# Kernel tuning notes

Hardware: AMD Instinct MI355X
Metric: run time of the kernel (lower is better)

The kernel has to match this reference:

```python
import jax, jax.numpy as jnp
import numpy as np

B, D = 512, 512
NOBJ, NWRD = 12, 16  # word_feat rows act as 'objects', object_feat rows as 'words' (arg swap in SentiGAT.forward)
N_OW = NOBJ + NWRD
EPS = 1e-12


def _with_self_loops(src, dst, n):
    return (np.concatenate([src, np.arange(n)]), np.concatenate([dst, np.arange(n)]))

_src = np.tile(np.arange(NOBJ), NWRD)                 # arange(n_obj).repeat(n_words) in torch == tile
_dst = np.repeat(np.arange(NWRD), NOBJ) + NOBJ        # repeat_interleave + offset
SRC_OW, DST_OW = map(jnp.asarray, _with_self_loops(_src, _dst, N_OW))

_E5 = np.array([[0,0,0,0,1,1,1,1,2,2,2,2,3,3,3,3,4,4,4,4],
                [1,2,3,4,0,2,3,4,0,1,3,4,0,1,2,4,0,1,2,3]])
SRC5, DST5 = map(jnp.asarray, _with_self_loops(_E5[0], _E5[1], 5))


def gat_conv(x, src, dst, W, a_src, a_dst, bias, concat, num_nodes):
    """PyG GATConv (add_self_loops already in src/dst, negative_slope=0.2, dropout=0)."""
    heads, out_dim = a_src.shape
    h = (x @ W).reshape(num_nodes, heads, out_dim)
    e = jax.nn.leaky_relu((h * a_src).sum(-1)[src] + (h * a_dst).sum(-1)[dst], 0.2)  # [E, heads]
    m = jax.ops.segment_max(e, dst, num_segments=num_nodes)
    p = jnp.exp(e - m[dst])
    alpha = p / jax.ops.segment_sum(p, dst, num_segments=num_nodes)[dst]             # softmax over incoming edges
    out = jax.ops.segment_sum(alpha[:, :, None] * h[src], dst, num_segments=num_nodes)
    out = out.reshape(num_nodes, heads * out_dim) if concat else out.mean(axis=1)
    return out + bias


def _ind_norm(f):
    # add_feature_indicator + F.normalize(p=2, dim=1, eps=1e-12)
    v = (f.sum(axis=1) != 0).astype(f.dtype)[:, None]
    g = jnp.concatenate([f, v], axis=1)
    return g / jnp.maximum(jnp.linalg.norm(g, axis=1, keepdims=True), EPS)


def setup_inputs() -> dict:
    k = jax.random.split(jax.random.key(0), 32)
    r = lambda i, s: jax.random.normal(k[i], s, dtype=jnp.float32)
    sc = 0.05
    return {
        "text_feat": r(0, (B, D)), "image_feat": r(1, (B, D)), "imgtxt_feat": r(2, (B, D)),
        "face_feat": r(3, (B, D)), "word_feat": r(4, (B, NOBJ, D)), "object_feat": r(5, (B, NWRD, D)),
        "ow_W": r(6, (D, 2 * D)) * sc, "ow_asrc": r(7, (2, D)) * sc, "ow_adst": r(8, (2, D)) * sc,
        "ow_b": jnp.zeros((D,), jnp.float32),
        "g1_W": r(9, (D + 1, D)) * sc, "g1_asrc": r(10, (1, D)) * sc, "g1_adst": r(11, (1, D)) * sc,
        "g1_b": jnp.zeros((D,), jnp.float32),
        "g2_W": r(12, (D, D)) * sc, "g2_asrc": r(13, (1, D)) * sc, "g2_adst": r(14, (1, D)) * sc,
        "g2_b": jnp.zeros((D,), jnp.float32),
        "m1_W": r(15, (5 * D, D)) * sc, "m1_b": jnp.zeros((D,), jnp.float32),
        "m2_W": r(16, (D, 3)) * sc, "m2_b": jnp.zeros((3,), jnp.float32),
    }


def reference(text_feat, image_feat, imgtxt_feat, face_feat, word_feat, object_feat,
              ow_W, ow_asrc, ow_adst, ow_b,
              g1_W, g1_asrc, g1_adst, g1_b,
              g2_W, g2_asrc, g2_adst, g2_b,
              m1_W, m1_b, m2_W, m2_b):
    # --- ObjectWordGAT (object_embs=word_feat, word_embs=object_feat per SentiGAT.forward) ---
    def per_sample(obj, wrd):
        x = jnp.concatenate([obj, wrd], axis=0)                       # [N_OW, D]
        h = gat_conv(x, SRC_OW, DST_OW, ow_W, ow_asrc, ow_adst, ow_b, False, N_OW)
        uo, uw = h[:NOBJ], h[NOBJ:]
        attn = jax.nn.softmax(uo @ uw.T, axis=1)                      # [NOBJ, NWRD]
        return (attn @ uw).mean(axis=0)                               # [D]
    aligned = jax.vmap(per_sample)(word_feat, object_feat)            # [B, D]

    feats = [_ind_norm(f) for f in (text_feat, image_feat, imgtxt_feat, face_feat, aligned)]
    x = jnp.stack(feats, axis=1)                                      # [B, 5, D+1]

    # edge_attr (cosine sims) is ignored by GATConv when edge_dim is None
    def graph5(xb):
        h = gat_conv(xb, SRC5, DST5, g1_W, g1_asrc, g1_adst, g1_b, True, 5)
        h = jax.nn.relu(h)
        return gat_conv(h, SRC5, DST5, g2_W, g2_asrc, g2_adst, g2_b, True, 5)
    x = jax.vmap(graph5)(x)                                           # [B, 5, D]

    fused = x.reshape(B, 5 * D)
    hid = jax.nn.relu(fused @ m1_W + m1_b)                            # dropout = identity (eval)
    return hid @ m2_W + m2_b                                          # [B, 3] logits
```

## Files before the change

### kernel.cpp

```cpp
#include <hip/hip_runtime.h>
#include <hip/hip_bf16.h>
#include <math.h>


#define B_SAMP 512

typedef short short8 __attribute__((ext_vector_type(8)));
typedef float floatx4 __attribute__((ext_vector_type(4)));

__device__ __forceinline__ float lrelu02(float x) { return x > 0.f ? x : 0.2f * x; }

__device__ __forceinline__ unsigned short cvt_bf16(float f) {
    union { float f; unsigned int u; } v; v.f = f;
    unsigned int u = v.u;
    return (unsigned short)((u + 0x7FFFu + ((u >> 16) & 1u)) >> 16);
}

__global__ __launch_bounds__(256) void prep(
    const float* __restrict__ ow_W, const float* __restrict__ ow_asrc,
    const float* __restrict__ ow_adst,
    const float* __restrict__ g1_W, const float* __restrict__ g2_W,
    const float* __restrict__ m1_W,
    float* __restrict__ vg, unsigned short* __restrict__ owWt,
    unsigned short* __restrict__ g1Wt, unsigned short* __restrict__ g2Wt,
    unsigned short* __restrict__ m1Wt)
{
    __shared__ float T[32][33];
    const int tid = threadIdx.x;
    int bid = blockIdx.x;

    if (bid < 128) {
        const int lane = tid & 63;
        const int gw = bid * 4 + (tid >> 6);
        for (int idx = gw; idx < 2048; idx += 512) {
            int t = idx >> 9, k = idx & 511;
            const float* a = (t < 2) ? (ow_asrc + t * 512) : (ow_adst + (t - 2) * 512);
            const float* wr = ow_W + (size_t)k * 1024 + (t & 1) * 512;
            float s = 0.f;
#pragma unroll
            for (int j = 0; j < 8; ++j) s += wr[lane + 64 * j] * a[lane + 64 * j];
            for (int off = 32; off > 0; off >>= 1) s += __shfl_down(s, off, 64);
            if (lane == 0) vg[idx] = s;
        }
        return;
    }
    bid -= 128;
    const float* W; int ldw, K, Kpad, koff, ktiles; float scale; unsigned short* Wt;
    if (bid < 256)        { W = ow_W;       ldw = 1024; K = 512;  Kpad = 1024; koff = 0;   scale = 0.5f; Wt = owWt; ktiles = 16; }
    else if (bid < 512)   { bid -= 256;  W = ow_W + 512; ldw = 1024; K = 512;  Kpad = 1024; koff = 512; scale = 0.5f; Wt = owWt; ktiles = 16; }
    else if (bid < 784)   { bid -= 512;  W = g1_W; ldw = 512; K = 513;  Kpad = 544;  koff = 0; scale = 1.f; Wt = g1Wt; ktiles = 17; }
    else if (bid < 1040)  { bid -= 784;  W = g2_W; ldw = 512; K = 512;  Kpad = 512;  koff = 0; scale = 1.f; Wt = g2Wt; ktiles = 16; }
    else                  { bid -= 1040; W = m1_W; ldw = 512; K = 2560; Kpad = 2560; koff = 0; scale = 1.f; Wt = m1Wt; ktiles = 80; }
    const int k0 = (bid % ktiles) * 32;
    const int n0 = (bid / ktiles) * 32;
    {
        int kr = tid >> 3, nc = (tid & 7) * 4;
        float4 v = make_float4(0.f, 0.f, 0.f, 0.f);
        if (k0 + kr < K) v = *(const float4*)(W + (size_t)(k0 + kr) * ldw + n0 + nc);
        T[nc + 0][kr] = v.x * scale; T[nc + 1][kr] = v.y * scale;
        T[nc + 2][kr] = v.z * scale; T[nc + 3][kr] = v.w * scale;
    }
    __syncthreads();
    {
        int nr = tid >> 3, kc = (tid & 7) * 4;
        ushort4 w;
        w.x = cvt_bf16(T[nr][kc + 0]);
        w.y = cvt_bf16(T[nr][kc + 1]);
        w.z = cvt_bf16(T[nr][kc + 2]);
        w.w = cvt_bf16(T[nr][kc + 3]);
        *(ushort4*)(Wt + (size_t)(n0 + nr) * Kpad + koff + k0 + kc) = w;
    }
}

__global__ __launch_bounds__(256) void ow_pre(
    const float* __restrict__ wf, const float* __restrict__ of,
    const float* __restrict__ vg,
    unsigned short* __restrict__ zcat)
{
    const int b = blockIdx.x;
    __shared__ float Xs[28][512];
    __shared__ float ss[28][2], sd[28][2];
    __shared__ float alpha[16][2][13];

    const int tid = threadIdx.x;
    const int lane = tid & 63;
    const int wid = tid >> 6;

    for (int idx = tid; idx < 28 * 128; idx += 256) {
        int n = idx >> 7, c = (idx & 127) * 4;
        const float* src = (n < 12) ? (wf + ((size_t)b * 12 + n) * 512)
                                    : (of + ((size_t)b * 16 + (n - 12)) * 512);
        *(float4*)&Xs[n][c] = *(const float4*)(src + c);
    }
    __syncthreads();

    for (int p = wid; p < 112; p += 4) {
        int n = p >> 2, t = p & 3;
        const float* vv = vg + t * 512;
        float s = 0.f;
#pragma unroll
        for (int j = 0; j < 8; ++j) s += Xs[n][lane + 64 * j] * vv[lane + 64 * j];
        for (int off = 32; off > 0; off >>= 1) s += __shfl_down(s, off, 64);
        if (lane == 0) { if (t < 2) ss[n][t] = s; else sd[n][t - 2] = s; }
    }
    __syncthreads();

    if (tid < 32) {
        int w = tid >> 1, h = tid & 1;
        float sdv = sd[12 + w][h];
        float e[13];
        float mx = -1e30f;
        for (int j = 0; j < 12; ++j) {
            e[j] = lrelu02(ss[j][h] + sdv);
            mx = fmaxf(mx, e[j]);
        }
        e[12] = lrelu02(ss[12 + w][h] + sdv);
        mx = fmaxf(mx, e[12]);
        float den = 0.f;
        for (int j = 0; j < 13; ++j) { e[j] = expf(e[j] - mx); den += e[j]; }
        float inv = 1.f / den;
        for (int j = 0; j < 13; ++j) alpha[w][h][j] = e[j] * inv;
    }
    __syncthreads();

    unsigned short* zb = zcat + (size_t)b * 28 * 1024;
    for (int idx = tid; idx < 12 * 1024; idx += 256) {
        int n = idx >> 10, d = idx & 511;
        zb[idx] = cvt_bf16(Xs[n][d]);
    }
    for (int c = tid; c < 1024; c += 256) {
        int h = c >> 9, d = c & 511;
        float xr[12];
#pragma unroll
        for (int j = 0; j < 12; ++j) xr[j] = Xs[j][d];
#pragma unroll 4
        for (int w = 0; w < 16; ++w) {
            float a = alpha[w][h][12] * Xs[12 + w][d];
#pragma unroll
            for (int j = 0; j < 12; ++j) a += alpha[w][h][j] * xr[j];
            zb[(size_t)(12 + w) * 1024 + c] = cvt_bf16(a);
        }
    }
}

template <int BM, int BN, int RELU, int SPLITK>
__global__ __launch_bounds__(256) void gemm_v2(
    const unsigned short* __restrict__ A, int lda,
    const unsigned short* __restrict__ Bt, int ldbt,
    float* __restrict__ C, int ldc,
    int M, int N, int K,
    const float* __restrict__ bias)
{
    constexpr int WM = BM / 2, WN = BN / 2;
    constexpr int MF = WM / 16, NF = WN / 16;
    constexpr int CA = BM / 64, CB = BN / 64;

    __shared__ unsigned short As[2][BM][40];
    __shared__ unsigned short Bs[2][BN][40];

    const int tid = threadIdx.x;
    const int m0 = blockIdx.x * BM;
    const int n0 = blockIdx.y * BN;
    const int lane = tid & 63;
    const int wid = tid >> 6;
    const int wm = (wid & 1) * WM;
    const int wn = (wid >> 1) * WN;
    const int fr = lane & 15;
    const int kq = (lane >> 4) * 8;

    const int srow = tid >> 2;
    const int scol = (tid & 3) * 8;

    const int kchunk = K / SPLITK;
    const int kbeg = (SPLITK > 1) ? blockIdx.z * kchunk : 0;
    const int kend = kbeg + kchunk;
    if (SPLITK > 1) C += (size_t)blockIdx.z * M * ldc;

    short8 ra[CA], rb[CB];
#define LOADAB(K0)                                                                   \
    do {                                                                             \
        _Pragma("unroll")                                                            \
        for (int c = 0; c < CA; ++c)                                                 \
            ra[c] = *(const short8*)(A + (size_t)(m0 + srow + c * 64) * lda + (K0) + scol); \
        _Pragma("unroll")                                                            \
        for (int c = 0; c < CB; ++c)                                                 \
            rb[c] = *(const short8*)(Bt + (size_t)(n0 + srow + c * 64) * ldbt + (K0) + scol); \
    } while (0)

    LOADAB(kbeg);

    floatx4 acc[MF][NF];
#pragma unroll
    for (int i = 0; i < MF; ++i)
#pragma unroll
        for (int j = 0; j < NF; ++j) acc[i][j] = (floatx4){0.f, 0.f, 0.f, 0.f};

    int t = 0;
    for (int k0 = kbeg; k0 < kend; k0 += 32, t ^= 1) {
#pragma unroll
        for (int c = 0; c < CA; ++c) *(short8*)&As[t][srow + c * 64][scol] = ra[c];
#pragma unroll
        for (int c = 0; c < CB; ++c) *(short8*)&Bs[t][srow + c * 64][scol] = rb[c];
        __syncthreads();
        if (k0 + 32 < kend) LOADAB(k0 + 32);

        short8 af[MF], bw[NF];
#pragma unroll
        for (int i = 0; i < MF; ++i)
            af[i] = *(const short8*)&As[t][wm + i * 16 + fr][kq];
#pragma unroll
        for (int j = 0; j < NF; ++j)
            bw[j] = *(const short8*)&Bs[t][wn + j * 16 + fr][kq];
#pragma unroll
        for (int i = 0; i < MF; ++i)
#pragma unroll
            for (int j = 0; j < NF; ++j)
                acc[i][j] = __builtin_amdgcn_mfma_f32_16x16x32_bf16(
                    af[i], bw[j], acc[i][j], 0, 0, 0);
    }
#undef LOADAB

    const int fq = lane >> 4;
#pragma unroll
    for (int i = 0; i < MF; ++i) {
#pragma unroll
        for (int j = 0; j < NF; ++j) {
#pragma unroll
            for (int q = 0; q < 4; ++q) {
                int row = m0 + wm + i * 16 + fq * 4 + q;
                int col = n0 + wn + j * 16 + fr;
                float v = acc[i][j][q];
                if (SPLITK == 1 && bias) v += bias[col];
                if (RELU) v = fmaxf(v, 0.f);
                C[(size_t)row * ldc + col] = v;
            }
        }
    }
}

__global__ __launch_bounds__(256) void attn_x5(
    const float* __restrict__ hout,
    const float* __restrict__ tf, const float* __restrict__ im,
    const float* __restrict__ it, const float* __restrict__ fa,
    unsigned short* __restrict__ x5)
{
    const int b = blockIdx.x;
    __shared__ float uo[12][520];
    __shared__ float uw[16][520];
    __shared__ float S[12][16];
    __shared__ float w16[16];
    __shared__ float al[512];

    const int tid = threadIdx.x;
    const int lane = tid & 63;
    const int wave = tid >> 6;
    const float* hb = hout + (size_t)b * 28 * 512;

    for (int idx = tid; idx < 28 * 128; idx += 256) {
        int n = idx >> 7, c = (idx & 127) * 4;
        float* row = (n < 12) ? &uo[n][0] : &uw[n - 12][0];
        *(float4*)&row[c] = *(const float4*)(hb + (size_t)n * 512 + c);
    }
    __syncthreads();

    if (tid < 192) {
        int i = tid >> 4, j = tid & 15;
        float s = 0.f;
        for (int d = 0; d < 128; ++d) {
            float4 a = *(const float4*)&uo[i][d * 4];
            float4 c = *(const float4*)&uw[j][d * 4];
            s += a.x * c.x + a.y * c.y + a.z * c.z + a.w * c.w;
        }
        S[i][j] = s;
    }
    __syncthreads();

    if (tid < 12) {
        float mx = -1e30f;
        for (int j = 0; j < 16; ++j) mx = fmaxf(mx, S[tid][j]);
        float den = 0.f;
        for (int j = 0; j < 16; ++j) { float p = expf(S[tid][j] - mx); S[tid][j] = p; den += p; }
        float inv = 1.f / den;
        for (int j = 0; j < 16; ++j) S[tid][j] *= inv;
    }
    __syncthreads();

    if (tid < 16) {
        float s = 0.f;
        for (int i = 0; i < 12; ++i) s += S[i][tid];
        w16[tid] = s * (1.f / 12.f);
    }
    __syncthreads();

    for (int d = tid; d < 512; d += 256) {
        float s = 0.f;
#pragma unroll
        for (int j = 0; j < 16; ++j) s += w16[j] * uw[j][d];
        al[d] = s;
    }
    __syncthreads();

    for (int f = wave; f < 5; f += 4) {
        const float* src = (f == 0) ? tf : (f == 1) ? im : (f == 2) ? it : (f == 3) ? fa : nullptr;
        float vals[8];
        float sum = 0.f, sq = 0.f;
#pragma unroll
        for (int j = 0; j < 8; ++j) {
            float v = (f < 4) ? src[(size_t)b * 512 + lane + 64 * j] : al[lane + 64 * j];
            vals[j] = v;
            sum += v;
            sq += v * v;
        }
#pragma unroll
        for (int off = 32; off > 0; off >>= 1) {
            sum += __shfl_xor(sum, off, 64);
            sq  += __shfl_xor(sq,  off, 64);
        }
        float v = (sum != 0.f) ? 1.f : 0.f;
        float nrm = fmaxf(sqrtf(sq + v * v), 1e-12f);
        float inv = 1.f / nrm;
        unsigned short* dst = x5 + ((size_t)b * 5 + f) * 544;
#pragma unroll
        for (int j = 0; j < 8; ++j) dst[lane + 64 * j] = cvt_bf16(vals[j] * inv);
        if (lane == 0) dst[512] = cvt_bf16(v * inv);
        else if (lane < 32) dst[512 + lane] = 0;
    }
}

template <int RELU>
__global__ __launch_bounds__(256) void g5_gat(
    const float* __restrict__ Hg,
    const float* __restrict__ asrc, const float* __restrict__ adst,
    const float* __restrict__ bias, unsigned short* __restrict__ outp)
{
    const int b = blockIdx.x;
    __shared__ float ss[5], sd[5];
    __shared__ float alpha[5][5];

    const int tid = threadIdx.x;
    const int lane = tid & 63;
    const int wave = tid >> 6;
    const float* Hb = Hg + (size_t)b * 5 * 512;

    for (int p = wave; p < 10; p += 4) {
        int n = p >> 1, ty = p & 1;
        const float* hv = Hb + n * 512;
        const float* av = ty ? adst : asrc;
        float s = 0.f;
#pragma unroll
        for (int j = 0; j < 8; ++j) s += hv[lane + 64 * j] * av[lane + 64 * j];
        for (int off = 32; off > 0; off >>= 1) s += __shfl_down(s, off, 64);
        if (lane == 0) { if (ty) sd[n] = s; else ss[n] = s; }
    }
    __syncthreads();

    if (tid < 5) {
        int dn = tid;
        float e[5];
        float mx = -1e30f;
        for (int s = 0; s < 5; ++s) {
            e[s] = lrelu02(ss[s] + sd[dn]);
            mx = fmaxf(mx, e[s]);
        }
        float den = 0.f;
        for (int s = 0; s < 5; ++s) { e[s] = expf(e[s] - mx); den += e[s]; }
        float inv = 1.f / den;
        for (int s = 0; s < 5; ++s) alpha[dn][s] = e[s] * inv;
    }
    __syncthreads();

    for (int d = tid; d < 512; d += 256) {
        float h0 = Hb[0 * 512 + d], h1 = Hb[1 * 512 + d], h2 = Hb[2 * 512 + d];
        float h3 = Hb[3 * 512 + d], h4 = Hb[4 * 512 + d];
        float bd = bias[d];
#pragma unroll
        for (int dn = 0; dn < 5; ++dn) {
            float v = alpha[dn][0] * h0 + alpha[dn][1] * h1 + alpha[dn][2] * h2 +
                      alpha[dn][3] * h3 + alpha[dn][4] * h4 + bd;
            if (RELU) v = fmaxf(v, 0.f);
            outp[((size_t)b * 5 + dn) * 512 + d] = cvt_bf16(v);
        }
    }
}

__global__ __launch_bounds__(64) void final2(
    const float* __restrict__ parts, const float* __restrict__ b1,
    const float* __restrict__ w, const float* __restrict__ bvec,
    float* __restrict__ out)
{
    const int b = blockIdx.x;
    const int lane = threadIdx.x;
    float a0 = 0.f, a1 = 0.f, a2 = 0.f;
#pragma unroll
    for (int j = 0; j < 8; ++j) {
        int d = lane + 64 * j;
        size_t o = (size_t)b * 512 + d;
        float x = parts[o] + parts[262144 + o] + parts[524288 + o] + parts[786432 + o] + b1[d];
        x = fmaxf(x, 0.f);
        a0 += x * w[d * 3 + 0];
        a1 += x * w[d * 3 + 1];
        a2 += x * w[d * 3 + 2];
    }
    for (int off = 32; off > 0; off >>= 1) {
        a0 += __shfl_down(a0, off, 64);
        a1 += __shfl_down(a1, off, 64);
        a2 += __shfl_down(a2, off, 64);
    }
    if (lane == 0) {
        out[b * 3 + 0] = a0 + bvec[0];
        out[b * 3 + 1] = a1 + bvec[1];
        out[b * 3 + 2] = a2 + bvec[2];
    }
}

extern "C" void kernel_launch(void* const* d_in, const int* in_sizes, int n_in,
                              void* d_out, int out_size, void* d_ws, size_t ws_size,
                              hipStream_t stream) {
    const float* text   = (const float*)d_in[0];
    const float* image  = (const float*)d_in[1];
    const float* imgtxt = (const float*)d_in[2];
    const float* face   = (const float*)d_in[3];
    const float* word   = (const float*)d_in[4];
    const float* obj    = (const float*)d_in[5];
    const float* ow_W    = (const float*)d_in[6];
    const float* ow_asrc = (const float*)d_in[7];
    const float* ow_adst = (const float*)d_in[8];
    const float* ow_b    = (const float*)d_in[9];
    const float* g1_W    = (const float*)d_in[10];
    const float* g1_asrc = (const float*)d_in[11];
    const float* g1_adst = (const float*)d_in[12];
    const float* g1_b    = (const float*)d_in[13];
    const float* g2_W    = (const float*)d_in[14];
    const float* g2_asrc = (const float*)d_in[15];
    const float* g2_adst = (const float*)d_in[16];
    const float* g2_b    = (const float*)d_in[17];
    const float* m1_W    = (const float*)d_in[18];
    const float* m1_b    = (const float*)d_in[19];
    const float* m2_W    = (const float*)d_in[20];
    const float* m2_b    = (const float*)d_in[21];

    float* ws = (float*)d_ws;
    float* vg = ws;
    unsigned short* owWt = (unsigned short*)(ws + 2048);
    unsigned short* g1Wt = owWt + 524288;
    unsigned short* g2Wt = g1Wt + 278528;
    unsigned short* m1Wt = g2Wt + 262144;
    unsigned short* zcat = m1Wt + 1310720;
    unsigned short* x5b  = zcat + 14680064;
    unsigned short* h1b  = x5b + 1392640;
    unsigned short* fsb  = h1b + 1310720;
    float* hout = (float*)(fsb + 1310720);
    float* hg   = hout + 7340032;
    float* hidp = hg + 1310720;

    prep<<<2448, 256, 0, stream>>>(ow_W, ow_asrc, ow_adst, g1_W, g2_W, m1_W,
                                   vg, owWt, g1Wt, g2Wt, m1Wt);

    ow_pre<<<B_SAMP, 256, 0, stream>>>(word, obj, vg, zcat);
    gemm_v2<128, 128, 0, 1><<<dim3(112, 4), 256, 0, stream>>>(
        zcat, 1024, owWt, 1024, hout, 512, 14336, 512, 1024, ow_b);
    attn_x5<<<B_SAMP, 256, 0, stream>>>(hout, text, image, imgtxt, face, x5b);

    gemm_v2<64, 64, 0, 1><<<dim3(40, 8), 256, 0, stream>>>(
        x5b, 544, g1Wt, 544, hg, 512, 2560, 512, 544, nullptr);
    g5_gat<1><<<B_SAMP, 256, 0, stream>>>(hg, g1_asrc, g1_adst, g1_b, h1b);
    gemm_v2<64, 64, 0, 1><<<dim3(40, 8), 256, 0, stream>>>(
        h1b, 512, g2Wt, 512, hg, 512, 2560, 512, 512, nullptr);
    g5_gat<0><<<B_SAMP, 256, 0, stream>>>(hg, g2_asrc, g2_adst, g2_b, fsb);

    gemm_v2<64, 64, 0, 4><<<dim3(8, 8, 4), 256, 0, stream>>>(
        fsb, 2560, m1Wt, 2560, hidp, 512, 512, 512, 2560, nullptr);
    final2<<<B_SAMP, 64, 0, stream>>>(hidp, m1_b, m2_W, m2_b, (float*)d_out);
}
```

Measured before the change: 126.9 us.

## Fuse object-word GAT preprocessing, projection GEMM and attention into one kernel

Replaces the ow_pre, 128x128 GEMM and attn_x5 kernels with one per-sample kernel. The aggregated features are kept in shared memory, each block runs the 28x1024 by 1024x512 projection with MFMA, and attention plus normalisation follow in place. This is meant to remove the global writes and reads of the large zcat and hout intermediates and two launches. In exchange every block streams the full projection weight, the large shared allocation limits occupancy to one block per CU, and the M dimension is padded from 28 to 32.

```diff
diff --git a/kernel.cpp b/kernel.cpp
--- a/kernel.cpp
+++ b/kernel.cpp
@@ -72,16 +72,21 @@
     }
 }
 
-__global__ __launch_bounds__(256) void ow_pre(
+__global__ __launch_bounds__(256) void fusedA(
     const float* __restrict__ wf, const float* __restrict__ of,
-    const float* __restrict__ vg,
-    unsigned short* __restrict__ zcat)
+    const float* __restrict__ vg, const unsigned short* __restrict__ Bt,
+    const float* __restrict__ ow_b,
+    const float* __restrict__ tf, const float* __restrict__ im,
+    const float* __restrict__ it, const float* __restrict__ fa,
+    unsigned short* __restrict__ x5)
 {
+    __shared__ __align__(16) char smem[156608];
+    float* Xs = (float*)smem;
+    unsigned short* Z = (unsigned short*)(smem + 57792);
+    char* BsB = smem + 123840;
+    float* sml = (float*)BsB;
+
     const int b = blockIdx.x;
-    __shared__ float Xs[28][512];
-    __shared__ float ss[28][2], sd[28][2];
-    __shared__ float alpha[16][2][13];
-
     const int tid = threadIdx.x;
     const int lane = tid & 63;
     const int wid = tid >> 6;
@@ -90,56 +95,184 @@
         int n = idx >> 7, c = (idx & 127) * 4;
         const float* src = (n < 12) ? (wf + ((size_t)b * 12 + n) * 512)
                                     : (of + ((size_t)b * 16 + (n - 12)) * 512);
-        *(float4*)&Xs[n][c] = *(const float4*)(src + c);
-    }
-    __syncthreads();
-
+        *(float4*)&Xs[n * 516 + c] = *(const float4*)(src + c);
+    }
+    __syncthreads();
+
+    float* ss = sml;
+    float* sd = sml + 56;
+    float* alpha = sml + 112;
     for (int p = wid; p < 112; p += 4) {
         int n = p >> 2, t = p & 3;
         const float* vv = vg + t * 512;
         float s = 0.f;
 #pragma unroll
-        for (int j = 0; j < 8; ++j) s += Xs[n][lane + 64 * j] * vv[lane + 64 * j];
+        for (int j = 0; j < 8; ++j) s += Xs[n * 516 + lane + 64 * j] * vv[lane + 64 * j];
         for (int off = 32; off > 0; off >>= 1) s += __shfl_down(s, off, 64);
-        if (lane == 0) { if (t < 2) ss[n][t] = s; else sd[n][t - 2] = s; }
-    }
-    __syncthreads();
-
+        if (lane == 0) { if (t < 2) ss[n * 2 + t] = s; else sd[n * 2 + t - 2] = s; }
+    }
+    __syncthreads();
     if (tid < 32) {
         int w = tid >> 1, h = tid & 1;
-        float sdv = sd[12 + w][h];
-        float e[13];
-        float mx = -1e30f;
-        for (int j = 0; j < 12; ++j) {
-            e[j] = lrelu02(ss[j][h] + sdv);
-            mx = fmaxf(mx, e[j]);
-        }
-        e[12] = lrelu02(ss[12 + w][h] + sdv);
-        mx = fmaxf(mx, e[12]);
+        float sdv = sd[(12 + w) * 2 + h];
+        float e[13], mx = -1e30f;
+        for (int j = 0; j < 12; ++j) { e[j] = lrelu02(ss[j * 2 + h] + sdv); mx = fmaxf(mx, e[j]); }
+        e[12] = lrelu02(ss[(12 + w) * 2 + h] + sdv); mx = fmaxf(mx, e[12]);
         float den = 0.f;
         for (int j = 0; j < 13; ++j) { e[j] = expf(e[j] - mx); den += e[j]; }
         float inv = 1.f / den;
-        for (int j = 0; j < 13; ++j) alpha[w][h][j] = e[j] * inv;
-    }
-    __syncthreads();
-
-    unsigned short* zb = zcat + (size_t)b * 28 * 1024;
+        for (int j = 0; j < 13; ++j) alpha[(w * 2 + h) * 13 + j] = e[j] * inv;
+    }
+    __syncthreads();
+
+    short8 rb[8];
+#pragma unroll
+    for (int i = 0; i < 8; ++i) {
+        int idx = tid + i * 256;
+        int row = idx >> 2, seg = idx & 3;
+        rb[i] = *(const short8*)(Bt + (size_t)row * 1024 + seg * 8);
+    }
+
     for (int idx = tid; idx < 12 * 1024; idx += 256) {
-        int n = idx >> 10, d = idx & 511;
-        zb[idx] = cvt_bf16(Xs[n][d]);
+        int n = idx >> 10, dd = idx & 1023;
+        Z[n * 1032 + dd] = cvt_bf16(Xs[n * 516 + (dd & 511)]);
     }
     for (int c = tid; c < 1024; c += 256) {
         int h = c >> 9, d = c & 511;
         float xr[12];
 #pragma unroll
-        for (int j = 0; j < 12; ++j) xr[j] = Xs[j][d];
+        for (int j = 0; j < 12; ++j) xr[j] = Xs[j * 516 + d];
 #pragma unroll 4
         for (int w = 0; w < 16; ++w) {
-            float a = alpha[w][h][12] * Xs[12 + w][d];
-#pragma unroll
-            for (int j = 0; j < 12; ++j) a += alpha[w][h][j] * xr[j];
-            zb[(size_t)(12 + w) * 1024 + c] = cvt_bf16(a);
-        }
+            const float* alp = &alpha[(w * 2 + h) * 13];
+            float a = alp[12] * Xs[(12 + w) * 516 + d];
+#pragma unroll
+            for (int j = 0; j < 12; ++j) a += alp[j] * xr[j];
+            Z[(12 + w) * 1032 + c] = cvt_bf16(a);
+        }
+    }
+    for (int idx = tid; idx < 4 * 1024; idx += 256)
+        Z[(28 + (idx >> 10)) * 1032 + (idx & 1023)] = 0;
+    __syncthreads();
+
+    const int wn = wid * 128;
+    const int fr = lane & 15;
+    const int slot = lane >> 4;
+    floatx4 acc[2][8];
+#pragma unroll
+    for (int i = 0; i < 2; ++i)
+#pragma unroll
+        for (int j = 0; j < 8; ++j) acc[i][j] = (floatx4){0.f, 0.f, 0.f, 0.f};
+
+    for (int k0 = 0; k0 < 1024; k0 += 32) {
+#pragma unroll
+        for (int i = 0; i < 8; ++i) {
+            int idx = tid + i * 256;
+            int row = idx >> 2, seg = idx & 3;
+            int sw = seg ^ ((row >> 2) & 3);
+            *(short8*)(BsB + row * 64 + sw * 16) = rb[i];
+        }
+        __syncthreads();
+        if (k0 + 32 < 1024) {
+#pragma unroll
+            for (int i = 0; i < 8; ++i) {
+                int idx = tid + i * 256;
+                int row = idx >> 2, seg = idx & 3;
+                rb[i] = *(const short8*)(Bt + (size_t)row * 1024 + (k0 + 32) + seg * 8);
+            }
+        }
+        short8 af[2];
+#pragma unroll
+        for (int i = 0; i < 2; ++i)
+            af[i] = *(const short8*)&Z[(i * 16 + fr) * 1032 + k0 + slot * 8];
+#pragma unroll
+        for (int j = 0; j < 8; ++j) {
+            int row = wn + j * 16 + fr;
+            int sw = slot ^ ((row >> 2) & 3);
+            short8 bw = *(const short8*)(BsB + row * 64 + sw * 16);
+#pragma unroll
+            for (int i = 0; i < 2; ++i)
+                acc[i][j] = __builtin_amdgcn_mfma_f32_16x16x32_bf16(af[i], bw, acc[i][j], 0, 0, 0);
+        }
+        __syncthreads();
+    }
+
+    const int fq = lane >> 4;
+#pragma unroll
+    for (int i = 0; i < 2; ++i) {
+#pragma unroll
+        for (int j = 0; j < 8; ++j) {
+#pragma unroll
+            for (int q = 0; q < 4; ++q) {
+                int row = i * 16 + fq * 4 + q;
+                int col = wn + j * 16 + fr;
+                if (row < 28) Xs[row * 516 + col] = acc[i][j][q] + ow_b[col];
+            }
+        }
+    }
+    __syncthreads();
+
+    float* S = sml;
+    float* w16 = sml + 192;
+    float* al = sml + 208;
+    if (tid < 192) {
+        int i = tid >> 4, j = tid & 15;
+        float s = 0.f;
+        for (int d = 0; d < 128; ++d) {
+            float4 a = *(const float4*)&Xs[i * 516 + d * 4];
+            float4 c = *(const float4*)&Xs[(12 + j) * 516 + d * 4];
+            s += a.x * c.x + a.y * c.y + a.z * c.z + a.w * c.w;
+        }
+        S[i * 16 + j] = s;
+    }
+    __syncthreads();
+    if (tid < 12) {
+        float mx = -1e30f;
+        for (int j = 0; j < 16; ++j) mx = fmaxf(mx, S[tid * 16 + j]);
+        float den = 0.f;
+        for (int j = 0; j < 16; ++j) { float p = expf(S[tid * 16 + j] - mx); S[tid * 16 + j] = p; den += p; }
+        float inv = 1.f / den;
+        for (int j = 0; j < 16; ++j) S[tid * 16 + j] *= inv;
+    }
+    __syncthreads();
+    if (tid < 16) {
+        float s = 0.f;
+        for (int i = 0; i < 12; ++i) s += S[i * 16 + tid];
+        w16[tid] = s * (1.f / 12.f);
+    }
+    __syncthreads();
+    for (int d = tid; d < 512; d += 256) {
+        float s = 0.f;
+#pragma unroll
+        for (int j = 0; j < 16; ++j) s += w16[j] * Xs[(12 + j) * 516 + d];
+        al[d] = s;
+    }
+    __syncthreads();
+
+    for (int f = wid; f < 5; f += 4) {
+        const float* src = (f == 0) ? tf : (f == 1) ? im : (f == 2) ? it : (f == 3) ? fa : nullptr;
+        float vals[8];
+        float sum = 0.f, sq = 0.f;
+#pragma unroll
+        for (int j = 0; j < 8; ++j) {
+            float v = (f < 4) ? src[(size_t)b * 512 + lane + 64 * j] : al[lane + 64 * j];
+            vals[j] = v;
+            sum += v;
+            sq += v * v;
+        }
+#pragma unroll
+        for (int off = 32; off > 0; off >>= 1) {
+            sum += __shfl_xor(sum, off, 64);
+            sq  += __shfl_xor(sq,  off, 64);
+        }
+        float v = (sum != 0.f) ? 1.f : 0.f;
+        float nrm = fmaxf(sqrtf(sq + v * v), 1e-12f);
+        float inv = 1.f / nrm;
+        unsigned short* dst = x5 + ((size_t)b * 5 + f) * 544;
+#pragma unroll
+        for (int j = 0; j < 8; ++j) dst[lane + 64 * j] = cvt_bf16(vals[j] * inv);
+        if (lane == 0) dst[512] = cvt_bf16(v * inv);
+        else if (lane < 32) dst[512 + lane] = 0;
     }
 }
 
@@ -235,95 +368,6 @@
                 C[(size_t)row * ldc + col] = v;
             }
         }
-    }
-}
-
-__global__ __launch_bounds__(256) void attn_x5(
-    const float* __restrict__ hout,
-    const float* __restrict__ tf, const float* __restrict__ im,
-    const float* __restrict__ it, const float* __restrict__ fa,
-    unsigned short* __restrict__ x5)
-{
-    const int b = blockIdx.x;
-    __shared__ float uo[12][520];
-    __shared__ float uw[16][520];
-    __shared__ float S[12][16];
-    __shared__ float w16[16];
-    __shared__ float al[512];
-
-    const int tid = threadIdx.x;
-    const int lane = tid & 63;
-    const int wave = tid >> 6;
-    const float* hb = hout + (size_t)b * 28 * 512;
-
-    for (int idx = tid; idx < 28 * 128; idx += 256) {
-        int n = idx >> 7, c = (idx & 127) * 4;
-        float* row = (n < 12) ? &uo[n][0] : &uw[n - 12][0];
-        *(float4*)&row[c] = *(const float4*)(hb + (size_t)n * 512 + c);
-    }
-    __syncthreads();
-
-    if (tid < 192) {
-        int i = tid >> 4, j = tid & 15;
-        float s = 0.f;
-        for (int d = 0; d < 128; ++d) {
-            float4 a = *(const float4*)&uo[i][d * 4];
-            float4 c = *(const float4*)&uw[j][d * 4];
-            s += a.x * c.x + a.y * c.y + a.z * c.z + a.w * c.w;
-        }
-        S[i][j] = s;
-    }
-    __syncthreads();
-
-    if (tid < 12) {
-        float mx = -1e30f;
-        for (int j = 0; j < 16; ++j) mx = fmaxf(mx, S[tid][j]);
-        float den = 0.f;
-        for (int j = 0; j < 16; ++j) { float p = expf(S[tid][j] - mx); S[tid][j] = p; den += p; }
-        float inv = 1.f / den;
-        for (int j = 0; j < 16; ++j) S[tid][j] *= inv;
-    }
-    __syncthreads();
-
-    if (tid < 16) {
-        float s = 0.f;
-        for (int i = 0; i < 12; ++i) s += S[i][tid];
-        w16[tid] = s * (1.f / 12.f);
-    }
-    __syncthreads();
-
-    for (int d = tid; d < 512; d += 256) {
-        float s = 0.f;
-#pragma unroll
-        for (int j = 0; j < 16; ++j) s += w16[j] * uw[j][d];
-        al[d] = s;
-    }
-    __syncthreads();
-
-    for (int f = wave; f < 5; f += 4) {
-        const float* src = (f == 0) ? tf : (f == 1) ? im : (f == 2) ? it : (f == 3) ? fa : nullptr;
-        float vals[8];
-        float sum = 0.f, sq = 0.f;
-#pragma unroll
-        for (int j = 0; j < 8; ++j) {
-            float v = (f < 4) ? src[(size_t)b * 512 + lane + 64 * j] : al[lane + 64 * j];
-            vals[j] = v;
-            sum += v;
-            sq += v * v;
-        }
-#pragma unroll
-        for (int off = 32; off > 0; off >>= 1) {
-            sum += __shfl_xor(sum, off, 64);
-            sq  += __shfl_xor(sq,  off, 64);
-        }
-        float v = (sum != 0.f) ? 1.f : 0.f;
-        float nrm = fmaxf(sqrtf(sq + v * v), 1e-12f);
-        float inv = 1.f / nrm;
-        unsigned short* dst = x5 + ((size_t)b * 5 + f) * 544;
-#pragma unroll
-        for (int j = 0; j < 8; ++j) dst[lane + 64 * j] = cvt_bf16(vals[j] * inv);
-        if (lane == 0) dst[512] = cvt_bf16(v * inv);
-        else if (lane < 32) dst[512 + lane] = 0;
     }
 }
 
@@ -445,21 +489,17 @@
     unsigned short* g1Wt = owWt + 524288;
     unsigned short* g2Wt = g1Wt + 278528;
     unsigned short* m1Wt = g2Wt + 262144;
-    unsigned short* zcat = m1Wt + 1310720;
-    unsigned short* x5b  = zcat + 14680064;
+    unsigned short* x5b  = m1Wt + 1310720;
     unsigned short* h1b  = x5b + 1392640;
     unsigned short* fsb  = h1b + 1310720;
-    float* hout = (float*)(fsb + 1310720);
-    float* hg   = hout + 7340032;
+    float* hg   = (float*)(fsb + 1310720);
     float* hidp = hg + 1310720;
 
     prep<<<2448, 256, 0, stream>>>(ow_W, ow_asrc, ow_adst, g1_W, g2_W, m1_W,
                                    vg, owWt, g1Wt, g2Wt, m1Wt);
 
-    ow_pre<<<B_SAMP, 256, 0, stream>>>(word, obj, vg, zcat);
-    gemm_v2<128, 128, 0, 1><<<dim3(112, 4), 256, 0, stream>>>(
-        zcat, 1024, owWt, 1024, hout, 512, 14336, 512, 1024, ow_b);
-    attn_x5<<<B_SAMP, 256, 0, stream>>>(hout, text, image, imgtxt, face, x5b);
+    fusedA<<<B_SAMP, 256, 0, stream>>>(word, obj, vg, owWt, ow_b,
+                                       text, image, imgtxt, face, x5b);
 
     gemm_v2<64, 64, 0, 1><<<dim3(40, 8), 256, 0, stream>>>(
         x5b, 544, g1Wt, 544, hg, 512, 2560, 512, 544, nullptr);
```

After: 150.8 us. 1.19x slower.

## Store GEMM outputs as bf16 and shrink GEMM tiles for more blocks

Applied to the files above, without the earlier changes.

Generalises the MFMA GEMM with a configurable wave layout and an optional bf16 output. The large ow GEMM and the two GAT GEMMs now write bf16 intermediates, which halves the bytes written and re-read by attn_x5 and g5_gat. Tiles shrink (64x128, 32x64) so each launch has more blocks to spread across the CUs. attn_x5's score dot products become wave-parallel shuffle reductions. The intermediates lose precision by being rounded to bf16.

```diff
diff --git a/kernel.cpp b/kernel.cpp
--- a/kernel.cpp
+++ b/kernel.cpp
@@ -14,6 +14,10 @@
     union { float f; unsigned int u; } v; v.f = f;
     unsigned int u = v.u;
     return (unsigned short)((u + 0x7FFFu + ((u >> 16) & 1u)) >> 16);
+}
+__device__ __forceinline__ float bf2f(unsigned short u) {
+    union { unsigned int u; float f; } v; v.u = ((unsigned int)u) << 16;
+    return v.f;
 }
 
 __global__ __launch_bounds__(256) void prep(
@@ -108,14 +112,9 @@
     if (tid < 32) {
         int w = tid >> 1, h = tid & 1;
         float sdv = sd[12 + w][h];
-        float e[13];
-        float mx = -1e30f;
-        for (int j = 0; j < 12; ++j) {
-            e[j] = lrelu02(ss[j][h] + sdv);
-            mx = fmaxf(mx, e[j]);
-        }
-        e[12] = lrelu02(ss[12 + w][h] + sdv);
-        mx = fmaxf(mx, e[12]);
+        float e[13], mx = -1e30f;
+        for (int j = 0; j < 12; ++j) { e[j] = lrelu02(ss[j][h] + sdv); mx = fmaxf(mx, e[j]); }
+        e[12] = lrelu02(ss[12 + w][h] + sdv); mx = fmaxf(mx, e[12]);
         float den = 0.f;
         for (int j = 0; j < 13; ++j) { e[j] = expf(e[j] - mx); den += e[j]; }
         float inv = 1.f / den;
@@ -143,17 +142,18 @@
     }
 }
 
-template <int BM, int BN, int RELU, int SPLITK>
-__global__ __launch_bounds__(256) void gemm_v2(
+template <int BM, int BN, int WGM, int RELU, int SPLITK, int OBF16>
+__global__ __launch_bounds__(256) void gemm_v3(
     const unsigned short* __restrict__ A, int lda,
     const unsigned short* __restrict__ Bt, int ldbt,
-    float* __restrict__ C, int ldc,
+    void* __restrict__ Cv, int ldc,
     int M, int N, int K,
     const float* __restrict__ bias)
 {
-    constexpr int WM = BM / 2, WN = BN / 2;
+    constexpr int WGN = 4 / WGM;
+    constexpr int WM = BM / WGM, WN = BN / WGN;
     constexpr int MF = WM / 16, NF = WN / 16;
-    constexpr int CA = BM / 64, CB = BN / 64;
+    constexpr int CA = (BM * 4 + 255) / 256, CB = (BN * 4 + 255) / 256;
 
     __shared__ unsigned short As[2][BM][40];
     __shared__ unsigned short Bs[2][BN][40];
@@ -163,28 +163,33 @@
     const int n0 = blockIdx.y * BN;
     const int lane = tid & 63;
     const int wid = tid >> 6;
-    const int wm = (wid & 1) * WM;
-    const int wn = (wid >> 1) * WN;
+    const int wm = (wid % WGM) * WM;
+    const int wn = (wid / WGM) * WN;
     const int fr = lane & 15;
     const int kq = (lane >> 4) * 8;
-
-    const int srow = tid >> 2;
-    const int scol = (tid & 3) * 8;
 
     const int kchunk = K / SPLITK;
     const int kbeg = (SPLITK > 1) ? blockIdx.z * kchunk : 0;
     const int kend = kbeg + kchunk;
-    if (SPLITK > 1) C += (size_t)blockIdx.z * M * ldc;
+    float* Cf = (float*)Cv;
+    unsigned short* Cb = (unsigned short*)Cv;
+    if (SPLITK > 1) Cf += (size_t)blockIdx.z * M * ldc;
 
     short8 ra[CA], rb[CB];
-#define LOADAB(K0)                                                                   \
-    do {                                                                             \
-        _Pragma("unroll")                                                            \
-        for (int c = 0; c < CA; ++c)                                                 \
-            ra[c] = *(const short8*)(A + (size_t)(m0 + srow + c * 64) * lda + (K0) + scol); \
-        _Pragma("unroll")                                                            \
-        for (int c = 0; c < CB; ++c)                                                 \
-            rb[c] = *(const short8*)(Bt + (size_t)(n0 + srow + c * 64) * ldbt + (K0) + scol); \
+#define LOADAB(K0)                                                                       \
+    do {                                                                                 \
+        _Pragma("unroll")                                                                \
+        for (int c = 0; c < CA; ++c) {                                                   \
+            int id = tid + c * 256;                                                      \
+            if (BM * 4 % 256 == 0 || id < BM * 4)                                        \
+                ra[c] = *(const short8*)(A + (size_t)(m0 + (id >> 2)) * lda + (K0) + (id & 3) * 8); \
+        }                                                                                \
+        _Pragma("unroll")                                                                \
+        for (int c = 0; c < CB; ++c) {                                                   \
+            int id = tid + c * 256;                                                      \
+            if (BN * 4 % 256 == 0 || id < BN * 4)                                        \
+                rb[c] = *(const short8*)(Bt + (size_t)(n0 + (id >> 2)) * ldbt + (K0) + (id & 3) * 8); \
+        }                                                                                \
     } while (0)
 
     LOADAB(kbeg);
@@ -198,9 +203,17 @@
     int t = 0;
     for (int k0 = kbeg; k0 < kend; k0 += 32, t ^= 1) {
 #pragma unroll
-        for (int c = 0; c < CA; ++c) *(short8*)&As[t][srow + c * 64][scol] = ra[c];
-#pragma unroll
-        for (int c = 0; c < CB; ++c) *(short8*)&Bs[t][srow + c * 64][scol] = rb[c];
+        for (int c = 0; c < CA; ++c) {
+            int id = tid + c * 256;
+            if (BM * 4 % 256 == 0 || id < BM * 4)
+                *(short8*)&As[t][id >> 2][(id & 3) * 8] = ra[c];
+        }
+#pragma unroll
+        for (int c = 0; c < CB; ++c) {
+            int id = tid + c * 256;
+            if (BN * 4 % 256 == 0 || id < BN * 4)
+                *(short8*)&Bs[t][id >> 2][(id & 3) * 8] = rb[c];
+        }
         __syncthreads();
         if (k0 + 32 < kend) LOADAB(k0 + 32);
 
@@ -232,14 +245,15 @@
                 float v = acc[i][j][q];
                 if (SPLITK == 1 && bias) v += bias[col];
                 if (RELU) v = fmaxf(v, 0.f);
-                C[(size_t)row * ldc + col] = v;
+                if (OBF16) Cb[(size_t)row * ldc + col] = cvt_bf16(v);
+                else       Cf[(size_t)row * ldc + col] = v;
             }
         }
     }
 }
 
 __global__ __launch_bounds__(256) void attn_x5(
-    const float* __restrict__ hout,
+    const unsigned short* __restrict__ hout,
     const float* __restrict__ tf, const float* __restrict__ im,
     const float* __restrict__ it, const float* __restrict__ fa,
     unsigned short* __restrict__ x5)
@@ -253,25 +267,27 @@
 
     const int tid = threadIdx.x;
     const int lane = tid & 63;
-    const int wave = tid >> 6;
-    const float* hb = hout + (size_t)b * 28 * 512;
-
-    for (int idx = tid; idx < 28 * 128; idx += 256) {
-        int n = idx >> 7, c = (idx & 127) * 4;
-        float* row = (n < 12) ? &uo[n][0] : &uw[n - 12][0];
-        *(float4*)&row[c] = *(const float4*)(hb + (size_t)n * 512 + c);
-    }
-    __syncthreads();
-
-    if (tid < 192) {
-        int i = tid >> 4, j = tid & 15;
+    const int wid = tid >> 6;
+    const unsigned short* hb = hout + (size_t)b * 28 * 512;
+
+    for (int idx = tid; idx < 28 * 64; idx += 256) {
+        int n = idx >> 6, c = (idx & 63) * 8;
+        short8 v = *(const short8*)(hb + (size_t)n * 512 + c);
+        float* row = (n < 12) ? &uo[n][c] : &uw[n - 12][c];
+#pragma unroll
+        for (int j = 0; j < 8; ++j) row[j] = bf2f((unsigned short)v[j]);
+    }
+    __syncthreads();
+
+    for (int p = wid; p < 192; p += 4) {
+        int i = p >> 4, j = p & 15;
+        const float* ua = &uo[i][lane * 8];
+        const float* uc = &uw[j][lane * 8];
         float s = 0.f;
-        for (int d = 0; d < 128; ++d) {
-            float4 a = *(const float4*)&uo[i][d * 4];
-            float4 c = *(const float4*)&uw[j][d * 4];
-            s += a.x * c.x + a.y * c.y + a.z * c.z + a.w * c.w;
-        }
-        S[i][j] = s;
+#pragma unroll
+        for (int d = 0; d < 8; ++d) s += ua[d] * uc[d];
+        for (int off = 32; off > 0; off >>= 1) s += __shfl_down(s, off, 64);
+        if (lane == 0) S[i][j] = s;
     }
     __syncthreads();
 
@@ -300,7 +316,7 @@
     }
     __syncthreads();
 
-    for (int f = wave; f < 5; f += 4) {
+    for (int f = wid; f < 5; f += 4) {
         const float* src = (f == 0) ? tf : (f == 1) ? im : (f == 2) ? it : (f == 3) ? fa : nullptr;
         float vals[8];
         float sum = 0.f, sq = 0.f;
@@ -329,7 +345,7 @@
 
 template <int RELU>
 __global__ __launch_bounds__(256) void g5_gat(
-    const float* __restrict__ Hg,
+    const unsigned short* __restrict__ Hg,
     const float* __restrict__ asrc, const float* __restrict__ adst,
     const float* __restrict__ bias, unsigned short* __restrict__ outp)
 {
@@ -340,15 +356,15 @@
     const int tid = threadIdx.x;
     const int lane = tid & 63;
     const int wave = tid >> 6;
-    const float* Hb = Hg + (size_t)b * 5 * 512;
+    const unsigned short* Hb = Hg + (size_t)b * 5 * 512;
 
     for (int p = wave; p < 10; p += 4) {
         int n = p >> 1, ty = p & 1;
-        const float* hv = Hb + n * 512;
+        const unsigned short* hv = Hb + n * 512;
         const float* av = ty ? adst : asrc;
         float s = 0.f;
 #pragma unroll
-        for (int j = 0; j < 8; ++j) s += hv[lane + 64 * j] * av[lane + 64 * j];
+        for (int j = 0; j < 8; ++j) s += bf2f(hv[lane + 64 * j]) * av[lane + 64 * j];
         for (int off = 32; off > 0; off >>= 1) s += __shfl_down(s, off, 64);
         if (lane == 0) { if (ty) sd[n] = s; else ss[n] = s; }
     }
@@ -370,8 +386,8 @@
     __syncthreads();
 
     for (int d = tid; d < 512; d += 256) {
-        float h0 = Hb[0 * 512 + d], h1 = Hb[1 * 512 + d], h2 = Hb[2 * 512 + d];
-        float h3 = Hb[3 * 512 + d], h4 = Hb[4 * 512 + d];
+        float h0 = bf2f(Hb[0 * 512 + d]), h1 = bf2f(Hb[1 * 512 + d]), h2 = bf2f(Hb[2 * 512 + d]);
+        float h3 = bf2f(Hb[3 * 512 + d]), h4 = bf2f(Hb[4 * 512 + d]);
         float bd = bias[d];
 #pragma unroll
         for (int dn = 0; dn < 5; ++dn) {
@@ -441,34 +457,34 @@
 
     float* ws = (float*)d_ws;
     float* vg = ws;
-    unsigned short* owWt = (unsigned short*)(ws + 2048);
+    float* hidp = ws + 2048;
+    unsigned short* owWt = (unsigned short*)(hidp + 1048576);
     unsigned short* g1Wt = owWt + 524288;
     unsigned short* g2Wt = g1Wt + 278528;
     unsigned short* m1Wt = g2Wt + 262144;
     unsigned short* zcat = m1Wt + 1310720;
-    unsigned short* x5b  = zcat + 14680064;
+    unsigned short* houtb = zcat + 14680064;
+    unsigned short* x5b  = houtb + 7340032;
     unsigned short* h1b  = x5b + 1392640;
     unsigned short* fsb  = h1b + 1310720;
-    float* hout = (float*)(fsb + 1310720);
-    float* hg   = hout + 7340032;
-    float* hidp = hg + 1310720;
+    unsigned short* hgb  = fsb + 1310720;
 
     prep<<<2448, 256, 0, stream>>>(ow_W, ow_asrc, ow_adst, g1_W, g2_W, m1_W,
                                    vg, owWt, g1Wt, g2Wt, m1Wt);
 
     ow_pre<<<B_SAMP, 256, 0, stream>>>(word, obj, vg, zcat);
-    gemm_v2<128, 128, 0, 1><<<dim3(112, 4), 256, 0, stream>>>(
-        zcat, 1024, owWt, 1024, hout, 512, 14336, 512, 1024, ow_b);
-    attn_x5<<<B_SAMP, 256, 0, stream>>>(hout, text, image, imgtxt, face, x5b);
-
-    gemm_v2<64, 64, 0, 1><<<dim3(40, 8), 256, 0, stream>>>(
-        x5b, 544, g1Wt, 544, hg, 512, 2560, 512, 544, nullptr);
-    g5_gat<1><<<B_SAMP, 256, 0, stream>>>(hg, g1_asrc, g1_adst, g1_b, h1b);
-    gemm_v2<64, 64, 0, 1><<<dim3(40, 8), 256, 0, stream>>>(
-        h1b, 512, g2Wt, 512, hg, 512, 2560, 512, 512, nullptr);
-    g5_gat<0><<<B_SAMP, 256, 0, stream>>>(hg, g2_asrc, g2_adst, g2_b, fsb);
-
-    gemm_v2<64, 64, 0, 4><<<dim3(8, 8, 4), 256, 0, stream>>>(
+    gemm_v3<64, 128, 2, 0, 1, 1><<<dim3(224, 4), 256, 0, stream>>>(
+        zcat, 1024, owWt, 1024, houtb, 512, 14336, 512, 1024, ow_b);
+    attn_x5<<<B_SAMP, 256, 0, stream>>>(houtb, text, image, imgtxt, face, x5b);
+
+    gemm_v3<32, 64, 1, 0, 1, 1><<<dim3(80, 8), 256, 0, stream>>>(
+        x5b, 544, g1Wt, 544, hgb, 512, 2560, 512, 544, nullptr);
+    g5_gat<1><<<B_SAMP, 256, 0, stream>>>(hgb, g1_asrc, g1_adst, g1_b, h1b);
+    gemm_v3<32, 64, 1, 0, 1, 1><<<dim3(80, 8), 256, 0, stream>>>(
+        h1b, 512, g2Wt, 512, hgb, 512, 2560, 512, 512, nullptr);
+    g5_gat<0><<<B_SAMP, 256, 0, stream>>>(hgb, g2_asrc, g2_adst, g2_b, fsb);
+
+    gemm_v3<32, 64, 1, 0, 4, 0><<<dim3(16, 8, 4), 256, 0, stream>>>(
         fsb, 2560, m1Wt, 2560, hidp, 512, 512, 512, 2560, nullptr);
     final2<<<B_SAMP, 64, 0, stream>>>(hidp, m1_b, m2_W, m2_b, (float*)d_out);
 }
```

Measured after the change: 135.3 us. 6.7% more time.
